# Kernel tuning notes

Measured on AMD Instinct MI355X. Metric: run time of the kernel, lower is better.

## Reference

```python
import jax, jax.numpy as jnp
import numpy as np

N, E, LE, C = 20000, 320000, 640000, 128
EPS = 1e-7  # GENConv message eps


def _ln(x, g, b):
    # torch.nn.LayerNorm, eps=1e-5
    m = jnp.mean(x, axis=-1, keepdims=True)
    v = jnp.var(x, axis=-1, keepdims=True)
    return (x - m) * jax.lax.rsqrt(v + 1e-5) * g + b


def _mlp(x, W1, b1, g, b, W2, b2):
    # GENConv MLP, num_layers=2, norm='layer': Linear -> LayerNorm -> ReLU -> Linear
    h = jax.nn.relu(_ln(x @ W1 + b1, g, b))
    return h @ W2 + b2


def _gen_deep(x, src, dst, edge_attr, num_nodes, p):
    # DeepGCNLayer 'res+': norm -> relu -> dropout(eval=identity) -> GENConv -> + x
    h = jax.nn.relu(_ln(x, p['pre_g'], p['pre_b']))
    # GENConv message: relu(x_j [+ edge_attr]) + eps
    msg = h[src]
    if edge_attr is not None:
        msg = msg + edge_attr
    msg = jax.nn.relu(msg) + EPS  # [E, C]
    # softmax aggregation per destination segment, per channel
    logits = msg * p['t']
    mx = jax.ops.segment_max(logits, dst, num_segments=num_nodes)
    alpha = jnp.exp(logits - mx[dst])
    denom = jax.ops.segment_sum(alpha, dst, num_segments=num_nodes)
    aggr = jax.ops.segment_sum(alpha * msg, dst, num_segments=num_nodes)
    aggr = aggr / jnp.where(denom == 0, 1.0, denom)
    out = aggr + h  # GENConv root skip: out + x_r
    out = _mlp(out, p['W1'], p['b1'], p['ln_g'], p['ln_b'], p['W2'], p['b2'])
    return x + out  # res+ residual


def setup_inputs() -> dict:
    key = jax.random.key(0)
    ks = iter(jax.random.split(key, 16))
    s = 0.05
    d = {}
    d['v_x'] = jax.random.normal(next(ks), (N, C), jnp.float32)
    d['e_x'] = jax.random.normal(next(ks), (E, C), jnp.float32)
    d['v_edge_index'] = jax.random.randint(next(ks), (2, E), 0, N)
    d['e_edge_index'] = jax.random.randint(next(ks), (2, LE), 0, E)
    for pfx in ('e_', 'n_'):
        d[pfx + 'pre_g'] = jnp.ones((C,), jnp.float32)
        d[pfx + 'pre_b'] = jnp.zeros((C,), jnp.float32)
        d[pfx + 't'] = jnp.array(1.0, jnp.float32)
        d[pfx + 'W1'] = jax.random.normal(next(ks), (C, 2 * C), jnp.float32) * s
        d[pfx + 'b1'] = jnp.zeros((2 * C,), jnp.float32)
        d[pfx + 'ln_g'] = jnp.ones((2 * C,), jnp.float32)
        d[pfx + 'ln_b'] = jnp.zeros((2 * C,), jnp.float32)
        d[pfx + 'W2'] = jax.random.normal(next(ks), (2 * C, C), jnp.float32) * s
        d[pfx + 'b2'] = jnp.zeros((C,), jnp.float32)
    return d


def reference(v_x, e_x, v_edge_index, e_edge_index,
              e_pre_g, e_pre_b, e_t, e_W1, e_b1, e_ln_g, e_ln_b, e_W2, e_b2,
              n_pre_g, n_pre_b, n_t, n_W1, n_b1, n_ln_g, n_ln_b, n_W2, n_b2):
    ep = dict(pre_g=e_pre_g, pre_b=e_pre_b, t=e_t, W1=e_W1, b1=e_b1,
              ln_g=e_ln_g, ln_b=e_ln_b, W2=e_W2, b2=e_b2)
    npar = dict(pre_g=n_pre_g, pre_b=n_pre_b, t=n_t, W1=n_W1, b1=n_b1,
                ln_g=n_ln_g, ln_b=n_ln_b, W2=n_W2, b2=n_b2)
    # edge layer: GENConv over the line graph (no edge_attr)
    e_out = _gen_deep(e_x, e_edge_index[0], e_edge_index[1], None, E, ep)
    # node layer: GENConv over node graph with updated edge features as edge_attr
    v_out = _gen_deep(v_x, v_edge_index[0], v_edge_index[1], e_out, N, npar)
    return (v_out, e_out)
```

## Files before the change

kernel.cpp:

```cpp
#include <hip/hip_runtime.h>
#include <hip/hip_bf16.h>

#define GEN_EPS 1e-7f

typedef __attribute__((ext_vector_type(8))) short short8;
typedef __attribute__((ext_vector_type(4))) float f32x4;

__global__ void ln_relu_kernel(const float* __restrict__ x, const float* __restrict__ g,
                               const float* __restrict__ b, __hip_bfloat16* __restrict__ h,
                               int M) {
  int lane = threadIdx.x & 63;
  int r = blockIdx.x * 4 + (threadIdx.x >> 6);
  if (r >= M) return;
  float2 v = ((const float2*)(x + (size_t)r * 128))[lane];
  float s = v.x + v.y;
#pragma unroll
  for (int o = 32; o; o >>= 1) s += __shfl_xor(s, o);
  float m = s * (1.0f / 128.0f);
  float dx = v.x - m, dy = v.y - m;
  float q = dx * dx + dy * dy;
#pragma unroll
  for (int o = 32; o; o >>= 1) q += __shfl_xor(q, o);
  float rstd = rsqrtf(q * (1.0f / 128.0f) + 1e-5f);
  float2 gv = ((const float2*)g)[lane], bv = ((const float2*)b)[lane];
  float2 hv;
  hv.x = fmaxf(fmaf(dx * rstd, gv.x, bv.x), 0.0f);
  hv.y = fmaxf(fmaf(dy * rstd, gv.y, bv.y), 0.0f);
  ((__hip_bfloat162*)(h + (size_t)r * 128))[lane] = __float22bfloat162_rn(hv);
}

__global__ void wprep_kernel(const float* __restrict__ W, short* __restrict__ WP,
                             int R, int Cc) {
  int c = blockIdx.x;
  size_t tbase = (size_t)(c >> 4) * (size_t)(16 * R);
  int rsub = c & 15;
  for (int k = threadIdx.x; k < R; k += blockDim.x) {
    __hip_bfloat16 bv = __float2bfloat16(W[(size_t)k * Cc + c]);
    int kk = k & 31;
    WP[tbase + (size_t)(k >> 5) * 512 + (kk >> 3) * 128 + rsub * 8 + (kk & 7)] =
        *(short*)&bv;
  }
}

__global__ void count_kernel(const int* __restrict__ dst, int* __restrict__ counts, int nnz) {
  int i = blockIdx.x * blockDim.x + threadIdx.x;
  if (i < nnz) atomicAdd(&counts[dst[i]], 1);
}

__global__ void scan_block_sums(const int* __restrict__ counts, int* __restrict__ bsums, int M) {
  __shared__ int sm[256];
  int t = threadIdx.x;
  int base = blockIdx.x * 1024 + t * 4;
  int s = 0;
#pragma unroll
  for (int i = 0; i < 4; i++) {
    int idx = base + i;
    if (idx < M) s += counts[idx];
  }
  sm[t] = s;
  __syncthreads();
  for (int o = 128; o; o >>= 1) {
    if (t < o) sm[t] += sm[t + o];
    __syncthreads();
  }
  if (t == 0) bsums[blockIdx.x] = sm[0];
}

__global__ void scan_bsums(int* bsums, int nb) {
  __shared__ int sm[512];
  int t = threadIdx.x;
  int v = (t < nb) ? bsums[t] : 0;
  sm[t] = v;
  __syncthreads();
  for (int o = 1; o < 512; o <<= 1) {
    int u = (t >= o) ? sm[t - o] : 0;
    __syncthreads();
    sm[t] += u;
    __syncthreads();
  }
  if (t < nb) bsums[t] = sm[t] - v;
}

__global__ void scan_write(const int* __restrict__ counts, const int* __restrict__ bsums,
                           int* __restrict__ off, int* __restrict__ cursor, int M, int nnz) {
  __shared__ int sm[256];
  int t = threadIdx.x;
  int base = blockIdx.x * 1024 + t * 4;
  int c[4];
  int s = 0;
#pragma unroll
  for (int i = 0; i < 4; i++) {
    int idx = base + i;
    c[i] = (idx < M) ? counts[idx] : 0;
    s += c[i];
  }
  sm[t] = s;
  __syncthreads();
  for (int o = 1; o < 256; o <<= 1) {
    int v = (t >= o) ? sm[t - o] : 0;
    __syncthreads();
    sm[t] += v;
    __syncthreads();
  }
  int p = bsums[blockIdx.x] + sm[t] - s;
#pragma unroll
  for (int i = 0; i < 4; i++) {
    int idx = base + i;
    if (idx < M) {
      off[idx] = p;
      cursor[idx] = p;
      p += c[i];
    }
  }
  if (blockIdx.x == 0 && t == 0) off[M] = nnz;
}

template <bool HAS_EID>
__global__ void fill_kernel(const int* __restrict__ src, const int* __restrict__ dst,
                            int* __restrict__ cursor, int* __restrict__ csr_src,
                            int* __restrict__ csr_eid, int nnz) {
  int i = blockIdx.x * blockDim.x + threadIdx.x;
  if (i >= nnz) return;
  int d = dst[i];
  int p = atomicAdd(&cursor[d], 1);
  csr_src[p] = src[i];
  if (HAS_EID) csr_eid[p] = i;
}

template <bool HAS_EATTR>
__global__ __launch_bounds__(256) void aggregate_kernel(
    const __hip_bfloat16* __restrict__ h, const int* __restrict__ off,
    const int* __restrict__ csr_src, const int* __restrict__ csr_eid,
    const ushort* __restrict__ eattr, const float* __restrict__ tptr,
    uint* __restrict__ yP, int M) {
  int lane = threadIdx.x & 63;
  int r = blockIdx.x * 4 + (threadIdx.x >> 6);
  if (r >= M) return;
  const float t = tptr[0];
  float2 hv = __bfloat1622float2(((const __hip_bfloat162*)(h + (size_t)r * 128))[lane]);
  int e0 = off[r], e1 = off[r + 1];
  float d0 = 0.0f, d1 = 0.0f, a0 = 0.0f, a1 = 0.0f;
  int sN = 0, idN = 0;
  if (e0 < e1) {
    sN = csr_src[e0];
    if (HAS_EATTR) idN = csr_eid[e0];
  }
  for (int e = e0; e < e1; e++) {
    int s = sN, id = idN;
    if (e + 1 < e1) {
      sN = csr_src[e + 1];
      if (HAS_EATTR) idN = csr_eid[e + 1];
    }
    float2 mv = __bfloat1622float2(((const __hip_bfloat162*)(h + (size_t)s * 128))[lane]);
    if (HAS_EATTR) {
      uint ea = ((const uint*)(eattr + (size_t)id * 128))[lane];
      float2 ef = __bfloat1622float2(*(__hip_bfloat162*)&ea);
      mv.x += ef.x;
      mv.y += ef.y;
    }
    float m0 = fmaxf(mv.x, 0.0f) + GEN_EPS;
    float m1 = fmaxf(mv.y, 0.0f) + GEN_EPS;
    float al0 = __expf(m0 * t), al1 = __expf(m1 * t);
    d0 += al0;
    d1 += al1;
    a0 = fmaf(al0, m0, a0);
    a1 = fmaf(al1, m1, a1);
  }
  float2 yv;
  yv.x = (e1 > e0 ? a0 / d0 : 0.0f) + hv.x;
  yv.y = (e1 > e0 ? a1 / d1 : 0.0f) + hv.y;
  __hip_bfloat162 yb2 = __float22bfloat162_rn(yv);
  yP[(r >> 4) * 1024 + (lane >> 4) * 256 + (r & 15) * 16 + (lane & 15)] = *(uint*)&yb2;
}

template <bool WRITE_BF16>
__global__ __launch_bounds__(512, 2) void mlp_kernel(
    const float* __restrict__ x, const short* yP, const short* __restrict__ W1P,
    const float* __restrict__ b1, const float* __restrict__ lng,
    const float* __restrict__ lnb, const short* __restrict__ W2P,
    const float* __restrict__ b2, float* __restrict__ out, ushort* out16,
    int ntiles, int stride, int M) {
  __shared__ short W1s[128 * 256];
  __shared__ short W2s[256 * 128];
  __shared__ short scr[8][2][16 * 34];

  const int tid = threadIdx.x, lane = tid & 63, wv = tid >> 6;
  const int rA = lane & 15, hi = lane >> 4;
  const int kA = hi * 8, jrow = hi * 4;
  const int foW = lane * 8;
  const int foA = rA * 32 + kA;

  {
    const short8* g1 = (const short8*)W1P;
    short8* l1 = (short8*)W1s;
#pragma unroll
    for (int i = 0; i < 8; i++) l1[i * 512 + tid] = g1[i * 512 + tid];
    const short8* g2 = (const short8*)W2P;
    short8* l2 = (short8*)W2s;
#pragma unroll
    for (int i = 0; i < 8; i++) l2[i * 512 + tid] = g2[i * 512 + tid];
  }

  float b1v[16], lngv[16], lnbv[16], b2v[8];
#pragma unroll
  for (int ct = 0; ct < 16; ct++) {
    int col = ct * 16 + rA;
    b1v[ct] = b1[col];
    lngv[ct] = lng[col];
    lnbv[ct] = lnb[col];
  }
#pragma unroll
  for (int ct = 0; ct < 8; ct++) b2v[ct] = b2[ct * 16 + rA];

  __syncthreads();

  int t = blockIdx.x * 8 + wv;
  short8 yA0, yA1, yA2, yA3;
  if (t < ntiles) {
    const short* yb = yP + (size_t)t * 2048 + foA;
    yA0 = *(const short8*)(yb);
    yA1 = *(const short8*)(yb + 512);
    yA2 = *(const short8*)(yb + 1024);
    yA3 = *(const short8*)(yb + 1536);
  }

  for (; t < ntiles; t += stride) {
    const int row0 = t * 16;

    f32x4 C1[16];
#pragma unroll
    for (int i = 0; i < 16; i++) C1[i] = (f32x4)0.0f;
#pragma unroll
    for (int kc = 0; kc < 4; kc++) {
      short8 a = (kc == 0) ? yA0 : (kc == 1) ? yA1 : (kc == 2) ? yA2 : yA3;
#pragma unroll
      for (int ct = 0; ct < 16; ct++) {
        short8 B = *(const short8*)&W1s[(ct * 4 + kc) * 512 + foW];
        C1[ct] = __builtin_amdgcn_mfma_f32_16x16x32_bf16(a, B, C1[ct], 0, 0, 0);
      }
    }

    {
      int tn = t + stride;
      int tc = (tn < ntiles) ? tn : t;
      const short* yb = yP + (size_t)tc * 2048 + foA;
      yA0 = *(const short8*)(yb);
      yA1 = *(const short8*)(yb + 512);
      yA2 = *(const short8*)(yb + 1024);
      yA3 = *(const short8*)(yb + 1536);
    }

    float xv[32];
#pragma unroll
    for (int ct = 0; ct < 8; ct++)
#pragma unroll
      for (int j = 0; j < 4; j++) {
        int row = row0 + jrow + j;
        int rr = (row < M) ? row : (M - 1);
        xv[ct * 4 + j] = x[(size_t)rr * 128 + ct * 16 + rA];
      }

#pragma unroll
    for (int ct = 0; ct < 16; ct++)
#pragma unroll
      for (int j = 0; j < 4; j++) C1[ct][j] += b1v[ct];

    float mean[4], rstd[4];
#pragma unroll
    for (int j = 0; j < 4; j++) {
      float p = 0.0f, q = 0.0f;
#pragma unroll
      for (int ct = 0; ct < 16; ct++) {
        p += C1[ct][j];
        q = fmaf(C1[ct][j], C1[ct][j], q);
      }
#pragma unroll
      for (int o = 1; o < 16; o <<= 1) {
        p += __shfl_xor(p, o);
        q += __shfl_xor(q, o);
      }
      float m = p * (1.0f / 256.0f);
      mean[j] = m;
      rstd[j] = rsqrtf(q * (1.0f / 256.0f) - m * m + 1e-5f);
    }

    f32x4 C2[8];
#pragma unroll
    for (int i = 0; i < 8; i++) C2[i] = (f32x4)0.0f;
#pragma unroll
    for (int kc = 0; kc < 8; kc++) {
      short* s = &scr[wv][kc & 1][0];
#pragma unroll
      for (int ct2 = 0; ct2 < 2; ct2++) {
        int ctg = kc * 2 + ct2;
#pragma unroll
        for (int j = 0; j < 4; j++) {
          float v =
              fmaxf(fmaf((C1[ctg][j] - mean[j]) * rstd[j], lngv[ctg], lnbv[ctg]), 0.0f);
          __hip_bfloat16 bv = __float2bfloat16(v);
          s[(jrow + j) * 34 + ct2 * 16 + rA] = *(short*)&bv;
        }
      }
      asm volatile("s_waitcnt lgkmcnt(0)" ::: "memory");
      __builtin_amdgcn_sched_barrier(0);
      short8 a = *(const short8*)&s[rA * 34 + kA];
#pragma unroll
      for (int ct = 0; ct < 8; ct++) {
        short8 B = *(const short8*)&W2s[(ct * 8 + kc) * 512 + foW];
        C2[ct] = __builtin_amdgcn_mfma_f32_16x16x32_bf16(a, B, C2[ct], 0, 0, 0);
      }
    }

#pragma unroll
    for (int ct = 0; ct < 8; ct++) {
#pragma unroll
      for (int j = 0; j < 4; j++) {
        int row = row0 + jrow + j;
        if (row < M) {
          size_t idx = (size_t)row * 128 + ct * 16 + rA;
          float o = C2[ct][j] + b2v[ct] + xv[ct * 4 + j];
          out[idx] = o;
          if (WRITE_BF16) {
            __hip_bfloat16 bo = __float2bfloat16(o);
            out16[idx] = *(ushort*)&bo;
          }
        }
      }
    }
  }
}

extern "C" void kernel_launch(void* const* d_in, const int* in_sizes, int n_in,
                              void* d_out, int out_size, void* d_ws, size_t ws_size,
                              hipStream_t stream) {
  const int C = 128;
  const float* v_x = (const float*)d_in[0];
  const float* e_x = (const float*)d_in[1];
  const int* v_ei = (const int*)d_in[2];
  const int* e_ei = (const int*)d_in[3];
  const int N = in_sizes[0] / C;
  const int E = in_sizes[1] / C;
  const int LE = in_sizes[3] / 2;

  const float* ep[9];
  const float* np_[9];
  for (int i = 0; i < 9; i++) ep[i] = (const float*)d_in[4 + i];
  for (int i = 0; i < 9; i++) np_[i] = (const float*)d_in[13 + i];

  float* v_out = (float*)d_out;
  float* e_out = (float*)d_out + (size_t)N * C;

  char* wsp = (char*)d_ws;
  size_t o = 0;
  auto carve = [&](size_t bytes) {
    void* p = wsp + o;
    o += (bytes + 255) & ~(size_t)255;
    return p;
  };
  short* yPe = (short*)carve((size_t)E * C * 2);
  short* yPn = (short*)carve((size_t)N * C * 2);
  int* counts = (int*)carve((size_t)E * 4);
  int* off = (int*)carve(((size_t)E + 1) * 4);
  int* cursor = (int*)carve((size_t)E * 4);
  int* bsums = (int*)carve(4096);
  int* csr_src = (int*)carve((size_t)LE * 4);
  int* csr_eid = (int*)carve((size_t)LE * 4);
  short* eW1P = (short*)carve((size_t)256 * 128 * 2);
  short* eW2P = (short*)carve((size_t)128 * 256 * 2);
  short* nW1P = (short*)carve((size_t)256 * 128 * 2);
  short* nW2P = (short*)carve((size_t)128 * 256 * 2);
  (void)ws_size;
  (void)n_in;
  (void)out_size;

  auto run_layer = [&](const float* x, const int* ei, int M, int nnz,
                       const ushort* eattr, const float** P, short* W1P, short* W2P,
                       short* yP, float* outp, ushort* out16) {
    const int* src = ei;
    const int* dst = ei + nnz;
    __hip_bfloat16* h = (__hip_bfloat16*)outp;
    hipMemsetAsync(counts, 0, (size_t)M * 4, stream);
    wprep_kernel<<<256, 128, 0, stream>>>(P[3], W1P, 128, 256);
    wprep_kernel<<<128, 256, 0, stream>>>(P[7], W2P, 256, 128);
    ln_relu_kernel<<<(M + 3) / 4, 256, 0, stream>>>(x, P[0], P[1], h, M);
    count_kernel<<<(nnz + 255) / 256, 256, 0, stream>>>(dst, counts, nnz);
    int nb = (M + 1023) / 1024;
    scan_block_sums<<<nb, 256, 0, stream>>>(counts, bsums, M);
    scan_bsums<<<1, 512, 0, stream>>>(bsums, nb);
    scan_write<<<nb, 256, 0, stream>>>(counts, bsums, off, cursor, M, nnz);
    if (eattr) {
      fill_kernel<true><<<(nnz + 255) / 256, 256, 0, stream>>>(src, dst, cursor, csr_src,
                                                               csr_eid, nnz);
      aggregate_kernel<true><<<(M + 3) / 4, 256, 0, stream>>>(h, off, csr_src, csr_eid,
                                                              eattr, P[2], (uint*)yP, M);
    } else {
      fill_kernel<false><<<(nnz + 255) / 256, 256, 0, stream>>>(src, dst, cursor, csr_src,
                                                                csr_eid, nnz);
      aggregate_kernel<false><<<(M + 3) / 4, 256, 0, stream>>>(h, off, csr_src, csr_eid,
                                                               nullptr, P[2], (uint*)yP, M);
    }
    int ntiles = (M + 15) / 16;
    int gblocks = (ntiles + 7) / 8;
    if (gblocks > 256) gblocks = 256;
    int stride = gblocks * 8;
    if (out16) {
      mlp_kernel<true><<<gblocks, 512, 0, stream>>>(x, yP, W1P, P[4], P[5], P[6], W2P,
                                                    P[8], outp, out16, ntiles, stride, M);
    } else {
      mlp_kernel<false><<<gblocks, 512, 0, stream>>>(x, yP, W1P, P[4], P[5], P[6], W2P,
                                                     P[8], outp, nullptr, ntiles, stride, M);
    }
  };

  run_layer(e_x, e_ei, E, LE, nullptr, ep, eW1P, eW2P, yPe, e_out, (ushort*)yPe);
  run_layer(v_x, v_ei, N, E, (const ushort*)yPe, np_, nW1P, nW2P, yPn, v_out, nullptr);
}
```

Baseline: 467.6 us.

## Batch both layers' preprocessing kernels and unroll the aggregation gather by four

Merges the per-layer weight prep, layernorm, degree count, scan and CSR fill kernels for the edge and node layers into single launches over both graphs, which roughly halves the number of small kernel launches and serial dependencies. The aggregation loop now gathers four neighbours per iteration, masking the ones past the segment end, so more independent loads are in flight per wave. The cost is extra branching in the merged kernels, separate CSR buffers per layer, and a little wasted work in partial groups of four.

New measurement: 442.7 us. 5.3% less time.

```diff
diff --git a/kernel.cpp b/kernel.cpp
--- a/kernel.cpp
+++ b/kernel.cpp
@@ -6,12 +6,25 @@
 typedef __attribute__((ext_vector_type(8))) short short8;
 typedef __attribute__((ext_vector_type(4))) float f32x4;
 
-__global__ void ln_relu_kernel(const float* __restrict__ x, const float* __restrict__ g,
-                               const float* __restrict__ b, __hip_bfloat16* __restrict__ h,
-                               int M) {
+__global__ void ln_relu_all(const float* __restrict__ ex, const float* __restrict__ vx,
+                            const float* __restrict__ eg, const float* __restrict__ eb,
+                            const float* __restrict__ ng, const float* __restrict__ nb_,
+                            __hip_bfloat16* __restrict__ he, __hip_bfloat16* __restrict__ hn,
+                            int E, int N) {
   int lane = threadIdx.x & 63;
-  int r = blockIdx.x * 4 + (threadIdx.x >> 6);
-  if (r >= M) return;
+  int rr = blockIdx.x * 4 + (threadIdx.x >> 6);
+  const float* x;
+  const float* g;
+  const float* b;
+  __hip_bfloat16* h;
+  int r;
+  if (rr < E) {
+    x = ex; g = eg; b = eb; h = he; r = rr;
+  } else if (rr < E + N) {
+    x = vx; g = ng; b = nb_; h = hn; r = rr - E;
+  } else {
+    return;
+  }
   float2 v = ((const float2*)(x + (size_t)r * 128))[lane];
   float s = v.x + v.y;
 #pragma unroll
@@ -29,9 +42,23 @@
   ((__hip_bfloat162*)(h + (size_t)r * 128))[lane] = __float22bfloat162_rn(hv);
 }
 
-__global__ void wprep_kernel(const float* __restrict__ W, short* __restrict__ WP,
-                             int R, int Cc) {
-  int c = blockIdx.x;
+__global__ void wprep_all(const float* __restrict__ eW1, const float* __restrict__ eW2,
+                          const float* __restrict__ nW1, const float* __restrict__ nW2,
+                          short* __restrict__ eW1P, short* __restrict__ eW2P,
+                          short* __restrict__ nW1P, short* __restrict__ nW2P) {
+  int b = blockIdx.x;
+  const float* W;
+  short* WP;
+  int R, Cc, c;
+  if (b < 256) {
+    W = eW1; WP = eW1P; R = 128; Cc = 256; c = b;
+  } else if (b < 384) {
+    W = eW2; WP = eW2P; R = 256; Cc = 128; c = b - 256;
+  } else if (b < 640) {
+    W = nW1; WP = nW1P; R = 128; Cc = 256; c = b - 384;
+  } else {
+    W = nW2; WP = nW2P; R = 256; Cc = 128; c = b - 640;
+  }
   size_t tbase = (size_t)(c >> 4) * (size_t)(16 * R);
   int rsub = c & 15;
   for (int k = threadIdx.x; k < R; k += blockDim.x) {
@@ -42,15 +69,29 @@
   }
 }
 
-__global__ void count_kernel(const int* __restrict__ dst, int* __restrict__ counts, int nnz) {
+__global__ void count_all(const int* __restrict__ e_dst, const int* __restrict__ v_dst,
+                          int* __restrict__ ce, int* __restrict__ cn, int LE, int En) {
   int i = blockIdx.x * blockDim.x + threadIdx.x;
-  if (i < nnz) atomicAdd(&counts[dst[i]], 1);
-}
-
-__global__ void scan_block_sums(const int* __restrict__ counts, int* __restrict__ bsums, int M) {
+  if (i < LE)
+    atomicAdd(&ce[e_dst[i]], 1);
+  else if (i < LE + En)
+    atomicAdd(&cn[v_dst[i - LE]], 1);
+}
+
+__global__ void scan_block_sums_all(const int* __restrict__ ce, const int* __restrict__ cn,
+                                    int* __restrict__ bsums, int nbE, int E, int N) {
   __shared__ int sm[256];
+  int b = blockIdx.x;
+  const int* counts;
+  int M, bb;
+  int* bs;
+  if (b < nbE) {
+    counts = ce; M = E; bb = b; bs = bsums;
+  } else {
+    counts = cn; M = N; bb = b - nbE; bs = bsums + 512;
+  }
   int t = threadIdx.x;
-  int base = blockIdx.x * 1024 + t * 4;
+  int base = bb * 1024 + t * 4;
   int s = 0;
 #pragma unroll
   for (int i = 0; i < 4; i++) {
@@ -63,13 +104,15 @@
     if (t < o) sm[t] += sm[t + o];
     __syncthreads();
   }
-  if (t == 0) bsums[blockIdx.x] = sm[0];
-}
-
-__global__ void scan_bsums(int* bsums, int nb) {
+  if (t == 0) bs[bb] = sm[0];
+}
+
+__global__ void scan_bsums_all(int* bsums, int nbE, int nbN) {
   __shared__ int sm[512];
+  int* bs = bsums + blockIdx.x * 512;
+  int nb = (blockIdx.x == 0) ? nbE : nbN;
   int t = threadIdx.x;
-  int v = (t < nb) ? bsums[t] : 0;
+  int v = (t < nb) ? bs[t] : 0;
   sm[t] = v;
   __syncthreads();
   for (int o = 1; o < 512; o <<= 1) {
@@ -78,14 +121,29 @@
     sm[t] += u;
     __syncthreads();
   }
-  if (t < nb) bsums[t] = sm[t] - v;
-}
-
-__global__ void scan_write(const int* __restrict__ counts, const int* __restrict__ bsums,
-                           int* __restrict__ off, int* __restrict__ cursor, int M, int nnz) {
+  if (t < nb) bs[t] = sm[t] - v;
+}
+
+__global__ void scan_write_all(const int* __restrict__ ce, const int* __restrict__ cn,
+                               const int* __restrict__ bsums, int* __restrict__ off_e,
+                               int* __restrict__ off_n, int* __restrict__ cur_e,
+                               int* __restrict__ cur_n, int nbE, int E, int N, int LE,
+                               int En) {
   __shared__ int sm[256];
+  int b = blockIdx.x;
+  const int* counts;
+  const int* bs;
+  int* off;
+  int* cursor;
+  int M, nnz, bb;
+  if (b < nbE) {
+    counts = ce; M = E; nnz = LE; bb = b; bs = bsums; off = off_e; cursor = cur_e;
+  } else {
+    counts = cn; M = N; nnz = En; bb = b - nbE; bs = bsums + 512; off = off_n;
+    cursor = cur_n;
+  }
   int t = threadIdx.x;
-  int base = blockIdx.x * 1024 + t * 4;
+  int base = bb * 1024 + t * 4;
   int c[4];
   int s = 0;
 #pragma unroll
@@ -102,7 +160,7 @@
     sm[t] += v;
     __syncthreads();
   }
-  int p = bsums[blockIdx.x] + sm[t] - s;
+  int p = bs[bb] + sm[t] - s;
 #pragma unroll
   for (int i = 0; i < 4; i++) {
     int idx = base + i;
@@ -112,19 +170,24 @@
       p += c[i];
     }
   }
-  if (blockIdx.x == 0 && t == 0) off[M] = nnz;
-}
-
-template <bool HAS_EID>
-__global__ void fill_kernel(const int* __restrict__ src, const int* __restrict__ dst,
-                            int* __restrict__ cursor, int* __restrict__ csr_src,
-                            int* __restrict__ csr_eid, int nnz) {
+  if (bb == 0 && t == 0) off[M] = nnz;
+}
+
+__global__ void fill_all(const int* __restrict__ e_src, const int* __restrict__ e_dst,
+                         const int* __restrict__ v_src, const int* __restrict__ v_dst,
+                         int* __restrict__ cur_e, int* __restrict__ cur_n,
+                         int* __restrict__ csrs_e, int* __restrict__ csrs_n,
+                         int* __restrict__ csre_n, int LE, int En) {
   int i = blockIdx.x * blockDim.x + threadIdx.x;
-  if (i >= nnz) return;
-  int d = dst[i];
-  int p = atomicAdd(&cursor[d], 1);
-  csr_src[p] = src[i];
-  if (HAS_EID) csr_eid[p] = i;
+  if (i < LE) {
+    int p = atomicAdd(&cur_e[e_dst[i]], 1);
+    csrs_e[p] = e_src[i];
+  } else if (i < LE + En) {
+    int j = i - LE;
+    int p = atomicAdd(&cur_n[v_dst[j]], 1);
+    csrs_n[p] = v_src[j];
+    csre_n[p] = j;
+  }
 }
 
 template <bool HAS_EATTR>
@@ -140,31 +203,37 @@
   float2 hv = __bfloat1622float2(((const __hip_bfloat162*)(h + (size_t)r * 128))[lane]);
   int e0 = off[r], e1 = off[r + 1];
   float d0 = 0.0f, d1 = 0.0f, a0 = 0.0f, a1 = 0.0f;
-  int sN = 0, idN = 0;
-  if (e0 < e1) {
-    sN = csr_src[e0];
-    if (HAS_EATTR) idN = csr_eid[e0];
-  }
-  for (int e = e0; e < e1; e++) {
-    int s = sN, id = idN;
-    if (e + 1 < e1) {
-      sN = csr_src[e + 1];
-      if (HAS_EATTR) idN = csr_eid[e + 1];
-    }
-    float2 mv = __bfloat1622float2(((const __hip_bfloat162*)(h + (size_t)s * 128))[lane]);
+  for (int e = e0; e < e1; e += 4) {
+    int n = e1 - e;
+    float2 mv[4];
+#pragma unroll
+    for (int u = 0; u < 4; u++) {
+      int ee = (u < n) ? e + u : e;
+      int s = csr_src[ee];
+      mv[u] = __bfloat1622float2(((const __hip_bfloat162*)(h + (size_t)s * 128))[lane]);
+    }
     if (HAS_EATTR) {
-      uint ea = ((const uint*)(eattr + (size_t)id * 128))[lane];
-      float2 ef = __bfloat1622float2(*(__hip_bfloat162*)&ea);
-      mv.x += ef.x;
-      mv.y += ef.y;
-    }
-    float m0 = fmaxf(mv.x, 0.0f) + GEN_EPS;
-    float m1 = fmaxf(mv.y, 0.0f) + GEN_EPS;
-    float al0 = __expf(m0 * t), al1 = __expf(m1 * t);
-    d0 += al0;
-    d1 += al1;
-    a0 = fmaf(al0, m0, a0);
-    a1 = fmaf(al1, m1, a1);
+#pragma unroll
+      for (int u = 0; u < 4; u++) {
+        int ee = (u < n) ? e + u : e;
+        int id = csr_eid[ee];
+        uint ea = ((const uint*)(eattr + (size_t)id * 128))[lane];
+        float2 ef = __bfloat1622float2(*(__hip_bfloat162*)&ea);
+        mv[u].x += ef.x;
+        mv[u].y += ef.y;
+      }
+    }
+#pragma unroll
+    for (int u = 0; u < 4; u++) {
+      float w = (u < n) ? 1.0f : 0.0f;
+      float m0 = fmaxf(mv[u].x, 0.0f) + GEN_EPS;
+      float m1 = fmaxf(mv[u].y, 0.0f) + GEN_EPS;
+      float al0 = __expf(m0 * t) * w, al1 = __expf(m1 * t) * w;
+      d0 += al0;
+      d1 += al1;
+      a0 = fmaf(al0, m0, a0);
+      a1 = fmaf(al1, m1, a1);
+    }
   }
   float2 yv;
   yv.x = (e1 > e0 ? a0 / d0 : 0.0f) + hv.x;
@@ -359,12 +428,15 @@
   };
   short* yPe = (short*)carve((size_t)E * C * 2);
   short* yPn = (short*)carve((size_t)N * C * 2);
-  int* counts = (int*)carve((size_t)E * 4);
-  int* off = (int*)carve(((size_t)E + 1) * 4);
-  int* cursor = (int*)carve((size_t)E * 4);
+  int* counts = (int*)carve((size_t)(E + N) * 4);
+  int* off_e = (int*)carve(((size_t)E + 1) * 4);
+  int* off_n = (int*)carve(((size_t)N + 1) * 4);
+  int* cur_e = (int*)carve((size_t)E * 4);
+  int* cur_n = (int*)carve((size_t)N * 4);
   int* bsums = (int*)carve(4096);
-  int* csr_src = (int*)carve((size_t)LE * 4);
-  int* csr_eid = (int*)carve((size_t)LE * 4);
+  int* csrs_e = (int*)carve((size_t)LE * 4);
+  int* csrs_n = (int*)carve((size_t)E * 4);
+  int* csre_n = (int*)carve((size_t)E * 4);
   short* eW1P = (short*)carve((size_t)256 * 128 * 2);
   short* eW2P = (short*)carve((size_t)128 * 256 * 2);
   short* nW1P = (short*)carve((size_t)256 * 128 * 2);
@@ -373,45 +445,48 @@
   (void)n_in;
   (void)out_size;
 
-  auto run_layer = [&](const float* x, const int* ei, int M, int nnz,
-                       const ushort* eattr, const float** P, short* W1P, short* W2P,
-                       short* yP, float* outp, ushort* out16) {
-    const int* src = ei;
-    const int* dst = ei + nnz;
-    __hip_bfloat16* h = (__hip_bfloat16*)outp;
-    hipMemsetAsync(counts, 0, (size_t)M * 4, stream);
-    wprep_kernel<<<256, 128, 0, stream>>>(P[3], W1P, 128, 256);
-    wprep_kernel<<<128, 256, 0, stream>>>(P[7], W2P, 256, 128);
-    ln_relu_kernel<<<(M + 3) / 4, 256, 0, stream>>>(x, P[0], P[1], h, M);
-    count_kernel<<<(nnz + 255) / 256, 256, 0, stream>>>(dst, counts, nnz);
-    int nb = (M + 1023) / 1024;
-    scan_block_sums<<<nb, 256, 0, stream>>>(counts, bsums, M);
-    scan_bsums<<<1, 512, 0, stream>>>(bsums, nb);
-    scan_write<<<nb, 256, 0, stream>>>(counts, bsums, off, cursor, M, nnz);
-    if (eattr) {
-      fill_kernel<true><<<(nnz + 255) / 256, 256, 0, stream>>>(src, dst, cursor, csr_src,
-                                                               csr_eid, nnz);
-      aggregate_kernel<true><<<(M + 3) / 4, 256, 0, stream>>>(h, off, csr_src, csr_eid,
-                                                              eattr, P[2], (uint*)yP, M);
-    } else {
-      fill_kernel<false><<<(nnz + 255) / 256, 256, 0, stream>>>(src, dst, cursor, csr_src,
-                                                                csr_eid, nnz);
-      aggregate_kernel<false><<<(M + 3) / 4, 256, 0, stream>>>(h, off, csr_src, csr_eid,
-                                                               nullptr, P[2], (uint*)yP, M);
-    }
-    int ntiles = (M + 15) / 16;
+  int* counts_e = counts;
+  int* counts_n = counts + E;
+  __hip_bfloat16* h_e = (__hip_bfloat16*)e_out;
+  __hip_bfloat16* h_n = (__hip_bfloat16*)v_out;
+
+  hipMemsetAsync(counts, 0, (size_t)(E + N) * 4, stream);
+  wprep_all<<<768, 256, 0, stream>>>(ep[3], ep[7], np_[3], np_[7], eW1P, eW2P, nW1P, nW2P);
+  ln_relu_all<<<(E + N + 3) / 4, 256, 0, stream>>>(e_x, v_x, ep[0], ep[1], np_[0], np_[1],
+                                                   h_e, h_n, E, N);
+  count_all<<<(LE + E + 255) / 256, 256, 0, stream>>>(e_ei + LE, v_ei + E, counts_e,
+                                                      counts_n, LE, E);
+  int nbE = (E + 1023) / 1024, nbN = (N + 1023) / 1024;
+  scan_block_sums_all<<<nbE + nbN, 256, 0, stream>>>(counts_e, counts_n, bsums, nbE, E, N);
+  scan_bsums_all<<<2, 512, 0, stream>>>(bsums, nbE, nbN);
+  scan_write_all<<<nbE + nbN, 256, 0, stream>>>(counts_e, counts_n, bsums, off_e, off_n,
+                                                cur_e, cur_n, nbE, E, N, LE, E);
+  fill_all<<<(LE + E + 255) / 256, 256, 0, stream>>>(e_ei, e_ei + LE, v_ei, v_ei + E,
+                                                     cur_e, cur_n, csrs_e, csrs_n, csre_n,
+                                                     LE, E);
+
+  aggregate_kernel<false><<<(E + 3) / 4, 256, 0, stream>>>(h_e, off_e, csrs_e, nullptr,
+                                                           nullptr, ep[2], (uint*)yPe, E);
+  {
+    int ntiles = (E + 15) / 16;
     int gblocks = (ntiles + 7) / 8;
     if (gblocks > 256) gblocks = 256;
     int stride = gblocks * 8;
-    if (out16) {
-      mlp_kernel<true><<<gblocks, 512, 0, stream>>>(x, yP, W1P, P[4], P[5], P[6], W2P,
-                                                    P[8], outp, out16, ntiles, stride, M);
-    } else {
-      mlp_kernel<false><<<gblocks, 512, 0, stream>>>(x, yP, W1P, P[4], P[5], P[6], W2P,
-                                                     P[8], outp, nullptr, ntiles, stride, M);
-    }
-  };
-
-  run_layer(e_x, e_ei, E, LE, nullptr, ep, eW1P, eW2P, yPe, e_out, (ushort*)yPe);
-  run_layer(v_x, v_ei, N, E, (const ushort*)yPe, np_, nW1P, nW2P, yPn, v_out, nullptr);
-}
+    mlp_kernel<true><<<gblocks, 512, 0, stream>>>(e_x, yPe, eW1P, ep[4], ep[5], ep[6],
+                                                  eW2P, ep[8], e_out, (ushort*)yPe,
+                                                  ntiles, stride, E);
+  }
+
+  aggregate_kernel<true><<<(N + 3) / 4, 256, 0, stream>>>(h_n, off_n, csrs_n, csre_n,
+                                                          (const ushort*)yPe, np_[2],
+                                                          (uint*)yPn, N);
+  {
+    int ntiles = (N + 15) / 16;
+    int gblocks = (ntiles + 7) / 8;
+    if (gblocks > 256) gblocks = 256;
+    int stride = gblocks * 8;
+    mlp_kernel<false><<<gblocks, 512, 0, stream>>>(v_x, yPn, nW1P, np_[4], np_[5], np_[6],
+                                                   nW2P, np_[8], v_out, nullptr, ntiles,
+                                                   stride, N);
+  }
+}
```
